# Performance work log

Hardware: AMD Instinct MI355X
Metric: run time of the kernel (lower is better)

## Reference

```python
import jax, jax.numpy as jnp
import numpy as np

N_NODES, N_EDGES = 50000, 800000
NODE_D, MSG_D, OUT_D = 128, 128, 128


def _linear_params(key, d_in, d_out):
    kw, _ = jax.random.split(key)
    W = jax.random.normal(kw, (d_in, d_out), jnp.float32) * np.float32(1.0 / np.sqrt(d_in))
    b = jnp.zeros((d_out,), jnp.float32)
    return W, b


def setup_inputs() -> dict:
    key = jax.random.key(0)
    ks = jax.random.split(key, 12)
    node_features = jax.random.normal(ks[0], (N_NODES, NODE_D), jnp.float32)
    src = jax.random.randint(ks[1], (N_EDGES,), 0, N_NODES, dtype=jnp.int32)
    dst = jax.random.randint(ks[2], (N_EDGES,), 0, N_NODES, dtype=jnp.int32)
    W_msg_1, b_msg_1 = _linear_params(ks[3], NODE_D, MSG_D)
    W_msg_2, b_msg_2 = _linear_params(ks[4], MSG_D, MSG_D)
    W_msg_3, b_msg_3 = _linear_params(ks[5], MSG_D, MSG_D)
    W_att_1, b_att_1 = _linear_params(ks[6], 2 * NODE_D, 1)
    W_att_2, b_att_2 = _linear_params(ks[7], 2 * NODE_D, 1)
    W_att_3, b_att_3 = _linear_params(ks[8], 2 * NODE_D, 1)
    W_c1, b_c1 = _linear_params(ks[9], MSG_D + NODE_D, OUT_D)
    W_c2, b_c2 = _linear_params(ks[10], OUT_D, OUT_D)
    return {
        'node_features': node_features, 'src': src, 'dst': dst,
        'W_msg_1': W_msg_1, 'b_msg_1': b_msg_1,
        'W_msg_2': W_msg_2, 'b_msg_2': b_msg_2,
        'W_msg_3': W_msg_3, 'b_msg_3': b_msg_3,
        'W_att_1': W_att_1, 'b_att_1': b_att_1,
        'W_att_2': W_att_2, 'b_att_2': b_att_2,
        'W_att_3': W_att_3, 'b_att_3': b_att_3,
        'W_c1': W_c1, 'b_c1': b_c1,
        'W_c2': W_c2, 'b_c2': b_c2,
    }


def reference(node_features, src, dst,
              W_msg_1, b_msg_1, W_msg_2, b_msg_2, W_msg_3, b_msg_3,
              W_att_1, b_att_1, W_att_2, b_att_2, W_att_3, b_att_3,
              W_c1, b_c1, W_c2, b_c2):
    # dropout(0.2) is identity in eval mode
    h = node_features                     # [N, D]
    N = h.shape[0]
    hs = h[src]                           # [E, D] gather source features
    hd = h[dst]                           # [E, D] gather dest features
    e = jnp.concatenate([hs, hd], axis=1)  # [E, 2D]

    # three per-edge scalar attention heads: exp(relu(linear))
    a1 = jnp.exp(jax.nn.relu(e @ W_att_1 + b_att_1))  # [E, 1]
    a2 = jnp.exp(jax.nn.relu(e @ W_att_2 + b_att_2))
    a3 = jnp.exp(jax.nn.relu(e @ W_att_3 + b_att_3))

    # per-destination normalizers (segment sums over incoming edges)
    att1 = jax.ops.segment_sum(a1, dst, num_segments=N)  # [N, 1]
    att2 = jax.ops.segment_sum(a2, dst, num_segments=N)
    att3 = jax.ops.segment_sum(a3, dst, num_segments=N)

    avg_a = (a1 / att1[dst] + a2 / att2[dst] + a3 / att3[dst]) / 3.0  # [E, 1]

    # gathered 3-layer MLP message, scaled by averaged attention
    m = avg_a * jax.nn.relu(
        jax.nn.relu(jax.nn.relu(hs @ W_msg_1 + b_msg_1) @ W_msg_2 + b_msg_2) @ W_msg_3 + b_msg_3
    )  # [E, M]

    # mean over incoming edges (nodes with no in-edges get 0, like DGL)
    deg = jax.ops.segment_sum(jnp.ones((src.shape[0], 1), h.dtype), dst, num_segments=N)
    h_neigh = jax.ops.segment_sum(m, dst, num_segments=N) / jnp.maximum(deg, 1.0)  # [N, M]

    hc = jnp.concatenate([h, h_neigh], axis=1)  # [N, D+M]
    out = jax.nn.relu(hc @ W_c1 + b_c1) @ W_c2 + b_c2  # [N, O]
    return out
```

## Files before the change

### kernel.cpp

```cpp
#include <hip/hip_runtime.h>

#define NDIM 128
#define NBKT 512
#define NWPART 128

typedef __attribute__((ext_vector_type(8))) short s8v;
typedef __attribute__((ext_vector_type(4))) float f4v;

__device__ inline unsigned short f2bf_rne(float x) {
    unsigned u = __float_as_uint(x);
    unsigned r = u + 0x7FFFu + ((u >> 16) & 1u);
    return (unsigned short)(r >> 16);
}
__device__ inline float bf2f(unsigned short b) {
    return __uint_as_float(((unsigned)b) << 16);
}

__global__ __launch_bounds__(256) void k_front(const float* __restrict__ h,
                                               const float* __restrict__ Wa1,
                                               const float* __restrict__ Wa2,
                                               const float* __restrict__ Wa3,
                                               float* __restrict__ proj,
                                               unsigned short* __restrict__ hb,
                                               const float* __restrict__ w0,
                                               const float* __restrict__ w1,
                                               const float* __restrict__ w2,
                                               const float* __restrict__ w3,
                                               const float* __restrict__ w4,
                                               const float* __restrict__ w5,
                                               unsigned short* __restrict__ wtout,
                                               const int* __restrict__ dst,
                                               int* __restrict__ hist,
                                               int N, int E, int npb)
{
    __shared__ int lh[NBKT];
    int tid = threadIdx.x;
    int nbProj = (N + 15) >> 4;
    int bid = blockIdx.x;

    if (bid < 384) {
        const float* srcs[6] = {w0, w1, w2, w3, w4, w5};
        int mat = bid >> 6;
        int idx = (bid & 63) * 256 + tid;
        int j    = idx & 7;
        int lane = (idx >> 3) & 63;
        int ks   = (idx >> 9) & 3;
        int ct   = idx >> 11;
        int col  = ct * 16 + (lane & 15);
        int k    = ks * 32 + (lane >> 4) * 8 + j;
        wtout[(size_t)mat * 16384 + idx] = f2bf_rne(srcs[mat][k * 128 + col]);
        return;
    }
    bid -= 384;
    if (bid < nbProj) {
        int l = tid & 15;
        int n = bid * 16 + (tid >> 4);
        if (n >= N) return;
        int o = l * 8;
        float4 w1s0 = *(const float4*)(Wa1 + o),       w1s1 = *(const float4*)(Wa1 + o + 4);
        float4 w1d0 = *(const float4*)(Wa1 + 128 + o), w1d1 = *(const float4*)(Wa1 + 132 + o);
        float4 w2s0 = *(const float4*)(Wa2 + o),       w2s1 = *(const float4*)(Wa2 + o + 4);
        float4 w2d0 = *(const float4*)(Wa2 + 128 + o), w2d1 = *(const float4*)(Wa2 + 132 + o);
        float4 w3s0 = *(const float4*)(Wa3 + o),       w3s1 = *(const float4*)(Wa3 + o + 4);
        float4 w3d0 = *(const float4*)(Wa3 + 128 + o), w3d1 = *(const float4*)(Wa3 + 132 + o);
        float4 x0 = *(const float4*)(h + (size_t)n * NDIM + o);
        float4 x1 = *(const float4*)(h + (size_t)n * NDIM + o + 4);
        {
            s8v hv;
            hv[0] = (short)f2bf_rne(x0.x); hv[1] = (short)f2bf_rne(x0.y);
            hv[2] = (short)f2bf_rne(x0.z); hv[3] = (short)f2bf_rne(x0.w);
            hv[4] = (short)f2bf_rne(x1.x); hv[5] = (short)f2bf_rne(x1.y);
            hv[6] = (short)f2bf_rne(x1.z); hv[7] = (short)f2bf_rne(x1.w);
            *(s8v*)(hb + (size_t)n * NDIM + o) = hv;
        }
        float s1 = x0.x*w1s0.x + x0.y*w1s0.y + x0.z*w1s0.z + x0.w*w1s0.w
                 + x1.x*w1s1.x + x1.y*w1s1.y + x1.z*w1s1.z + x1.w*w1s1.w;
        float s2 = x0.x*w2s0.x + x0.y*w2s0.y + x0.z*w2s0.z + x0.w*w2s0.w
                 + x1.x*w2s1.x + x1.y*w2s1.y + x1.z*w2s1.z + x1.w*w2s1.w;
        float s3 = x0.x*w3s0.x + x0.y*w3s0.y + x0.z*w3s0.z + x0.w*w3s0.w
                 + x1.x*w3s1.x + x1.y*w3s1.y + x1.z*w3s1.z + x1.w*w3s1.w;
        float d1 = x0.x*w1d0.x + x0.y*w1d0.y + x0.z*w1d0.z + x0.w*w1d0.w
                 + x1.x*w1d1.x + x1.y*w1d1.y + x1.z*w1d1.z + x1.w*w1d1.w;
        float d2 = x0.x*w2d0.x + x0.y*w2d0.y + x0.z*w2d0.z + x0.w*w2d0.w
                 + x1.x*w2d1.x + x1.y*w2d1.y + x1.z*w2d1.z + x1.w*w2d1.w;
        float d3 = x0.x*w3d0.x + x0.y*w3d0.y + x0.z*w3d0.z + x0.w*w3d0.w
                 + x1.x*w3d1.x + x1.y*w3d1.y + x1.z*w3d1.z + x1.w*w3d1.w;
#pragma unroll
        for (int m = 1; m < 16; m <<= 1) {
            s1 += __shfl_xor(s1, m);
            s2 += __shfl_xor(s2, m);
            s3 += __shfl_xor(s3, m);
            d1 += __shfl_xor(d1, m);
            d2 += __shfl_xor(d2, m);
            d3 += __shfl_xor(d3, m);
        }
        if (l == 0) {
            *(float4*)(proj + (size_t)n * 8)     = make_float4(s1, s2, s3, 0.f);
            *(float4*)(proj + (size_t)n * 8 + 4) = make_float4(d1, d2, d3, 0.f);
        }
        return;
    }
    bid -= nbProj;
    {
        int w = bid, NW = NWPART;
        for (int i = tid; i < NBKT; i += 256) lh[i] = 0;
        __syncthreads();
        int per = (E + NW - 1) / NW;
        int e0 = w * per, e1 = min(E, e0 + per);
        for (int e = e0 + tid; e < e1; e += 256)
            atomicAdd(&lh[dst[e] / npb], 1);
        __syncthreads();
        for (int b = tid; b < NBKT; b += 256)
            hist[b * NW + w] = lh[b];
    }
}

__global__ __launch_bounds__(NWPART) void k_pscan_a(int* __restrict__ hist,
                                                    int* __restrict__ tot)
{
    __shared__ int s[NWPART];
    int b = blockIdx.x, t = threadIdx.x;
    int v = hist[b * NWPART + t];
    s[t] = v;
    __syncthreads();
    for (int d = 1; d < NWPART; d <<= 1) {
        int u = (t >= d) ? s[t - d] : 0;
        __syncthreads();
        s[t] += u;
        __syncthreads();
    }
    hist[b * NWPART + t] = s[t] - v;
    if (t == NWPART - 1) tot[b] = s[NWPART - 1];
}

__global__ __launch_bounds__(NBKT) void k_pscan_b(const int* __restrict__ tot,
                                                  int* __restrict__ bbase, int E)
{
    __shared__ int s[NBKT];
    int b = threadIdx.x;
    int v = tot[b];
    s[b] = v;
    __syncthreads();
    for (int d = 1; d < NBKT; d <<= 1) {
        int u = (b >= d) ? s[b - d] : 0;
        __syncthreads();
        s[b] += u;
        __syncthreads();
    }
    bbase[b] = s[b] - v;
    if (b == NBKT - 1) bbase[NBKT] = E;
}


__device__ inline void g_pass_global(const unsigned short* __restrict__ A, int N, int row0,
                                     int ln, int g, int lane, int cw,
                                     const unsigned short* __restrict__ wf, f4v acc[2][2])
{
#pragma unroll
    for (int ks = 0; ks < 4; ++ks) {
        s8v a[2];
#pragma unroll
        for (int fr = 0; fr < 2; ++fr) {
            int rA = min(row0 + fr * 16 + ln, N - 1);
            a[fr] = *(const s8v*)(A + (size_t)rA * 128 + ks * 32 + g * 8);
        }
#pragma unroll
        for (int ct2 = 0; ct2 < 2; ++ct2) {
            int ct = cw * 2 + ct2;
            s8v wv = *(const s8v*)(wf + ((((ct << 2) + ks) * 64) + lane) * 8);
#pragma unroll
            for (int fr = 0; fr < 2; ++fr)
                acc[fr][ct2] = __builtin_amdgcn_mfma_f32_16x16x32_bf16(a[fr], wv, acc[fr][ct2], 0, 0, 0);
        }
    }
}

__device__ inline void g_pass_lds(const unsigned short* __restrict__ act,
                                  int rw, int ln, int g, int lane, int cw,
                                  const unsigned short* __restrict__ wf, f4v acc[2][2])
{
#pragma unroll
    for (int ks = 0; ks < 4; ++ks) {
        s8v a[2];
#pragma unroll
        for (int fr = 0; fr < 2; ++fr) {
            int rl = rw * 32 + fr * 16 + ln;
            a[fr] = *(const s8v*)(&act[(rl * 128 + ks * 32 + g * 8) ^ ((ln & 7) << 3)]);
        }
#pragma unroll
        for (int ct2 = 0; ct2 < 2; ++ct2) {
            int ct = cw * 2 + ct2;
            s8v wv = *(const s8v*)(wf + ((((ct << 2) + ks) * 64) + lane) * 8);
#pragma unroll
            for (int fr = 0; fr < 2; ++fr)
                acc[fr][ct2] = __builtin_amdgcn_mfma_f32_16x16x32_bf16(a[fr], wv, acc[fr][ct2], 0, 0, 0);
        }
    }
}

__device__ inline void write_act(f4v acc[2][2], const float* __restrict__ bias,
                                 unsigned short* __restrict__ act,
                                 int rw, int cw, int ln, int g)
{
#pragma unroll
    for (int ct2 = 0; ct2 < 2; ++ct2) {
        int col = (cw * 2 + ct2) * 16 + ln;
        float bv = bias[col];
#pragma unroll
        for (int fr = 0; fr < 2; ++fr) {
#pragma unroll
            for (int q = 0; q < 4; ++q) {
                int rl = rw * 32 + fr * 16 + g * 4 + q;
                float o = fmaxf(acc[fr][ct2][q] + bv, 0.f);
                act[(rl * 128 + col) ^ ((rl & 7) << 3)] = f2bf_rne(o);
                acc[fr][ct2][q] = 0.f;
            }
        }
    }
}

__global__ __launch_bounds__(512) void k_mid(const int* __restrict__ src,
                                             const int* __restrict__ dst,
                                             const int* __restrict__ hist,
                                             const int* __restrict__ bbase,
                                             unsigned* __restrict__ ebuf,
                                             int E, int npb,
                                             const unsigned short* __restrict__ hb,
                                             const unsigned short* __restrict__ w1,
                                             const unsigned short* __restrict__ w2,
                                             const unsigned short* __restrict__ w3,
                                             const float* __restrict__ b1,
                                             const float* __restrict__ b2,
                                             const float* __restrict__ b3,
                                             unsigned short* __restrict__ msg, int N)
{
    __shared__ int cur[NBKT];
    __shared__ unsigned short act0[8192];
    __shared__ unsigned short act1[8192];
    int tid = threadIdx.x;

    if (blockIdx.x < NWPART) {
        int w = blockIdx.x, NW = NWPART;
        for (int i = tid; i < NBKT; i += 512)
            cur[i] = hist[i * NW + w] + bbase[i];
        __syncthreads();
        int per = (E + NW - 1) / NW;
        int e0 = w * per, e1 = min(E, e0 + per);
        for (int e = e0 + tid; e < e1; e += 512) {
            int d = dst[e], b = d / npb;
            int pos = atomicAdd(&cur[b], 1);
            ebuf[pos] = ((unsigned)src[e] << 7) | (unsigned)(d - b * npb);
        }
        return;
    }
    int mb   = blockIdx.x - NWPART;
    int lane = tid & 63;
    int wid  = tid >> 6;
    int rw   = wid >> 2;
    int cw   = wid & 3;
    int ln   = lane & 15;
    int g    = lane >> 4;
    int row0 = mb * 64 + rw * 32;

    f4v acc[2][2] = {};
    g_pass_global(hb, N, row0, ln, g, lane, cw, w1, acc);
    write_act(acc, b1, act0, rw, cw, ln, g);
    __syncthreads();
    g_pass_lds(act0, rw, ln, g, lane, cw, w2, acc);
    write_act(acc, b2, act1, rw, cw, ln, g);
    __syncthreads();
    g_pass_lds(act1, rw, ln, g, lane, cw, w3, acc);
    write_act(acc, b3, act0, rw, cw, ln, g);
    __syncthreads();
#pragma unroll
    for (int i = 0; i < 2; ++i) {
        int id  = tid + 512 * i;
        int row = id >> 4;
        int c8  = (id & 15) * 8;
        int grow = mb * 64 + row;
        if (grow < N) {
            s8v v = *(const s8v*)(&act0[(row * 128 + c8) ^ ((row & 7) << 3)]);
            *(s8v*)(msg + (size_t)grow * 128 + c8) = v;
        }
    }
}

__global__ __launch_bounds__(256) void k_bucket(const unsigned* __restrict__ ebuf,
                                                const int* __restrict__ bbase,
                                                int* __restrict__ offs,
                                                int* __restrict__ perm,
                                                int N, int npb, int E)
{
    __shared__ int lc[128];
    __shared__ int ls[128];
    int b   = blockIdx.x;
    int tid = threadIdx.x;
    for (int i = tid; i < 128; i += 256) lc[i] = 0;
    __syncthreads();
    int e0 = bbase[b], e1 = bbase[b + 1];
    for (int e = e0 + tid; e < e1; e += 256)
        atomicAdd(&lc[ebuf[e] & 127], 1);
    __syncthreads();
    if (tid < 128) ls[tid] = lc[tid];
    __syncthreads();
    for (int d = 1; d < 128; d <<= 1) {
        int u = (tid < 128 && tid >= d) ? ls[tid - d] : 0;
        __syncthreads();
        if (tid < 128) ls[tid] += u;
        __syncthreads();
    }
    int n0 = b * npb;
    if (tid < 128) {
        int excl = ls[tid] - lc[tid] + e0;
        if (tid < npb && n0 + tid < N) offs[n0 + tid] = excl;
        lc[tid] = excl;
    }
    if (b == 0 && tid == 0) offs[N] = E;
    __syncthreads();
    for (int e = e0 + tid; e < e1; e += 256) {
        unsigned r = ebuf[e];
        int pos = atomicAdd(&lc[r & 127], 1);
        perm[pos] = (int)(r >> 7);
    }
}

__global__ __launch_bounds__(512) void k_tail(const unsigned short* __restrict__ hb,
                                              const unsigned short* __restrict__ msgb,
                                              const float* __restrict__ proj,
                                              const int* __restrict__ offs,
                                              const int* __restrict__ perm,
                                              const float* __restrict__ ba1,
                                              const float* __restrict__ ba2,
                                              const float* __restrict__ ba3,
                                              const unsigned short* __restrict__ wc1a,
                                              const unsigned short* __restrict__ wc1b,
                                              const unsigned short* __restrict__ wc2,
                                              const float* __restrict__ bc1,
                                              const float* __restrict__ bc2,
                                              float* __restrict__ out, int N)
{
    __shared__ unsigned short hn[8192];
    __shared__ unsigned short act0[8192];
    int tid  = threadIdx.x;
    int lane = tid & 63;
    int l    = lane & 15;
    int grp  = lane >> 4;
    int wv   = tid >> 6;
    int r0   = blockIdx.x * 64;
    float b1 = ba1[0], b2 = ba2[0], b3 = ba3[0];

    for (int rnd = 0; rnd < 2; ++rnd) {
        int rl = rnd * 32 + wv * 4 + grp;
        int n  = r0 + rl;
        bool alive = (n < N);
        int o0 = 0, o1 = 0;
        float dd1 = 0.f, dd2 = 0.f, dd3 = 0.f;
        if (alive) {
            o0 = offs[n];
            o1 = offs[n + 1];
            dd1 = proj[(size_t)n * 8 + 4];
            dd2 = proj[(size_t)n * 8 + 5];
            dd3 = proj[(size_t)n * 8 + 6];
        }
        int deg = o1 - o0;

        int   m0 = min(deg, 16);
        int   sc = 0;
        float a1c = 0.f, a2c = 0.f, a3c = 0.f;
        if (l < m0) {
            sc = perm[o0 + l];
            float4 sp = *(const float4*)(proj + (size_t)sc * 8);
            a1c = __expf(fmaxf(sp.x + dd1 + b1, 0.f));
            a2c = __expf(fmaxf(sp.y + dd2 + b2, 0.f));
            a3c = __expf(fmaxf(sp.z + dd3 + b3, 0.f));
        }
        float s1 = a1c, s2 = a2c, s3 = a3c;
        for (int i = o0 + 16 + l; i < o1; i += 16) {
            int s = perm[i];
            float4 sp = *(const float4*)(proj + (size_t)s * 8);
            s1 += __expf(fmaxf(sp.x + dd1 + b1, 0.f));
            s2 += __expf(fmaxf(sp.y + dd2 + b2, 0.f));
            s3 += __expf(fmaxf(sp.z + dd3 + b3, 0.f));
        }
#pragma unroll
        for (int m = 1; m < 16; m <<= 1) {
            s1 += __shfl_xor(s1, m);
            s2 += __shfl_xor(s2, m);
            s3 += __shfl_xor(s3, m);
        }
        float r1 = 1.f / s1, r2 = 1.f / s2, r3 = 1.f / s3;

        float acc[8] = {};
        int gbase = grp << 4;
        {
            float wvv = (a1c * r1 + a2c * r2 + a3c * r3) * (1.f / 3.f);
            for (int j = 0; j < m0; ++j) {
                int   s = __shfl(sc, gbase + j);
                float w = __shfl(wvv, gbase + j);
                s8v v = *(const s8v*)(msgb + (size_t)s * NDIM + l * 8);
#pragma unroll
                for (int k = 0; k < 8; ++k)
                    acc[k] += w * bf2f((unsigned short)v[k]);
            }
        }
        for (int base = o0 + 16; base < o1; base += 16) {
            int m  = min(16, o1 - base);
            int sv = 0;
            float wvv = 0.f;
            if (l < m) {
                sv = perm[base + l];
                float4 sp = *(const float4*)(proj + (size_t)sv * 8);
                float a1 = __expf(fmaxf(sp.x + dd1 + b1, 0.f));
                float a2 = __expf(fmaxf(sp.y + dd2 + b2, 0.f));
                float a3 = __expf(fmaxf(sp.z + dd3 + b3, 0.f));
                wvv = (a1 * r1 + a2 * r2 + a3 * r3) * (1.f / 3.f);
            }
            for (int j = 0; j < m; ++j) {
                int   s = __shfl(sv, gbase + j);
                float w = __shfl(wvv, gbase + j);
                s8v v = *(const s8v*)(msgb + (size_t)s * NDIM + l * 8);
#pragma unroll
                for (int k = 0; k < 8; ++k)
                    acc[k] += w * bf2f((unsigned short)v[k]);
            }
        }
        float inv = (alive && deg > 0) ? 1.f / (float)deg : 0.f;
        s8v hv;
#pragma unroll
        for (int k = 0; k < 8; ++k)
            hv[k] = (short)f2bf_rne(acc[k] * inv);
        *(s8v*)(&hn[(rl * 128 + l * 8) ^ ((rl & 7) << 3)]) = hv;
    }
    __syncthreads();

    int wid  = tid >> 6;
    int rw   = wid >> 2;
    int cw   = wid & 3;
    int ln   = lane & 15;
    int g    = lane >> 4;
    int row0 = r0 + rw * 32;

    f4v acc2[2][2] = {};
    g_pass_global(hb, N, row0, ln, g, lane, cw, wc1a, acc2);
    g_pass_lds(hn, rw, ln, g, lane, cw, wc1b, acc2);
    write_act(acc2, bc1, act0, rw, cw, ln, g);
    __syncthreads();
    g_pass_lds(act0, rw, ln, g, lane, cw, wc2, acc2);
#pragma unroll
    for (int ct2 = 0; ct2 < 2; ++ct2) {
        int col = (cw * 2 + ct2) * 16 + ln;
        float bv = bc2[col];
#pragma unroll
        for (int fr = 0; fr < 2; ++fr) {
#pragma unroll
            for (int q = 0; q < 4; ++q) {
                int orow = row0 + fr * 16 + g * 4 + q;
                if (orow < N)
                    out[(size_t)orow * 128 + col] = acc2[fr][ct2][q] + bv;
            }
        }
    }
}

extern "C" void kernel_launch(void* const* d_in, const int* in_sizes, int n_in,
                              void* d_out, int out_size, void* d_ws, size_t ws_size,
                              hipStream_t stream)
{
    const float* h   = (const float*)d_in[0];
    const int*   src = (const int*)d_in[1];
    const int*   dst = (const int*)d_in[2];
    const float* Wm1 = (const float*)d_in[3];
    const float* bm1 = (const float*)d_in[4];
    const float* Wm2 = (const float*)d_in[5];
    const float* bm2 = (const float*)d_in[6];
    const float* Wm3 = (const float*)d_in[7];
    const float* bm3 = (const float*)d_in[8];
    const float* Wa1 = (const float*)d_in[9];
    const float* ba1 = (const float*)d_in[10];
    const float* Wa2 = (const float*)d_in[11];
    const float* ba2 = (const float*)d_in[12];
    const float* Wa3 = (const float*)d_in[13];
    const float* ba3 = (const float*)d_in[14];
    const float* Wc1 = (const float*)d_in[15];
    const float* bc1 = (const float*)d_in[16];
    const float* Wc2 = (const float*)d_in[17];
    const float* bc2 = (const float*)d_in[18];

    const int N = in_sizes[0] / NDIM;
    const int E = in_sizes[1];
    const int npb = (N + NBKT - 1) / NBKT;
    float* out = (float*)d_out;

    unsigned short* wt  = (unsigned short*)d_ws;
    unsigned short* hb  = wt + 6 * 16384;
    unsigned short* mb2 = hb + (size_t)N * NDIM;
    float* proj = (float*)(mb2 + (size_t)N * NDIM);
    int* offs   = (int*)(proj + (size_t)N * 8);
    int* hist   = offs + N + 1;
    int* bbase  = hist + NBKT * NWPART;
    int* btot   = bbase + NBKT + 1;
    unsigned* ebuf = (unsigned*)(btot + NBKT);
    int* perm   = (int*)(ebuf + E);

    const unsigned short* wt_m1  = wt;
    const unsigned short* wt_m2  = wt + 1 * 16384;
    const unsigned short* wt_m3  = wt + 2 * 16384;
    const unsigned short* wt_c1a = wt + 3 * 16384;
    const unsigned short* wt_c1b = wt + 4 * 16384;
    const unsigned short* wt_c2  = wt + 5 * 16384;

    int nbProj = (N + 15) / 16;
    int gb64   = (N + 63) / 64;

    k_front<<<384 + nbProj + NWPART, 256, 0, stream>>>(
        h, Wa1, Wa2, Wa3, proj, hb,
        Wm1, Wm2, Wm3, Wc1, Wc1 + 128 * 128, Wc2, wt,
        dst, hist, N, E, npb);

    k_pscan_a<<<NBKT, NWPART, 0, stream>>>(hist, btot);
    k_pscan_b<<<1, NBKT, 0, stream>>>(btot, bbase, E);

    k_mid<<<NWPART + gb64, 512, 0, stream>>>(
        src, dst, hist, bbase, ebuf, E, npb,
        hb, wt_m1, wt_m2, wt_m3, bm1, bm2, bm3, mb2, N);

    k_bucket<<<NBKT, 256, 0, stream>>>(ebuf, bbase, offs, perm, N, npb, E);

    k_tail<<<gb64, 512, 0, stream>>>(
        hb, mb2, proj, offs, perm, ba1, ba2, ba3,
        wt_c1a, wt_c1b, wt_c2, bc1, bc2, out, N);
}
```

Before: 108.7 us.

## Align dst buckets to 64-node tiles and fuse per-node sort into tail kernel

```diff
diff --git a/kernel.cpp b/kernel.cpp
--- a/kernel.cpp
+++ b/kernel.cpp
@@ -1,8 +1,8 @@
 #include <hip/hip_runtime.h>
 
 #define NDIM 128
-#define NBKT 512
 #define NWPART 128
+#define MAXBKT 1024
 
 typedef __attribute__((ext_vector_type(8))) short s8v;
 typedef __attribute__((ext_vector_type(4))) float f4v;
@@ -31,9 +31,9 @@
                                                unsigned short* __restrict__ wtout,
                                                const int* __restrict__ dst,
                                                int* __restrict__ hist,
-                                               int N, int E, int npb)
-{
-    __shared__ int lh[NBKT];
+                                               int N, int E, int nbkt)
+{
+    __shared__ int lh[MAXBKT];
     int tid = threadIdx.x;
     int nbProj = (N + 15) >> 4;
     int bid = blockIdx.x;
@@ -103,14 +103,14 @@
     bid -= nbProj;
     {
         int w = bid, NW = NWPART;
-        for (int i = tid; i < NBKT; i += 256) lh[i] = 0;
+        for (int i = tid; i < nbkt; i += 256) lh[i] = 0;
         __syncthreads();
         int per = (E + NW - 1) / NW;
         int e0 = w * per, e1 = min(E, e0 + per);
         for (int e = e0 + tid; e < e1; e += 256)
-            atomicAdd(&lh[dst[e] / npb], 1);
-        __syncthreads();
-        for (int b = tid; b < NBKT; b += 256)
+            atomicAdd(&lh[dst[e] >> 6], 1);
+        __syncthreads();
+        for (int b = tid; b < nbkt; b += 256)
             hist[b * NW + w] = lh[b];
     }
 }
@@ -133,22 +133,23 @@
     if (t == NWPART - 1) tot[b] = s[NWPART - 1];
 }
 
-__global__ __launch_bounds__(NBKT) void k_pscan_b(const int* __restrict__ tot,
-                                                  int* __restrict__ bbase, int E)
-{
-    __shared__ int s[NBKT];
+__global__ __launch_bounds__(MAXBKT) void k_pscan_b(const int* __restrict__ tot,
+                                                    int* __restrict__ bbase,
+                                                    int E, int nbkt)
+{
+    __shared__ int s[MAXBKT];
     int b = threadIdx.x;
-    int v = tot[b];
+    int v = (b < nbkt) ? tot[b] : 0;
     s[b] = v;
     __syncthreads();
-    for (int d = 1; d < NBKT; d <<= 1) {
+    for (int d = 1; d < MAXBKT; d <<= 1) {
         int u = (b >= d) ? s[b - d] : 0;
         __syncthreads();
         s[b] += u;
         __syncthreads();
     }
-    bbase[b] = s[b] - v;
-    if (b == NBKT - 1) bbase[NBKT] = E;
+    if (b < nbkt) bbase[b] = s[b] - v;
+    if (b == nbkt - 1) bbase[nbkt] = E;
 }
 
 
@@ -224,7 +225,7 @@
                                              const int* __restrict__ hist,
                                              const int* __restrict__ bbase,
                                              unsigned* __restrict__ ebuf,
-                                             int E, int npb,
+                                             int E, int nbkt,
                                              const unsigned short* __restrict__ hb,
                                              const unsigned short* __restrict__ w1,
                                              const unsigned short* __restrict__ w2,
@@ -234,22 +235,22 @@
                                              const float* __restrict__ b3,
                                              unsigned short* __restrict__ msg, int N)
 {
-    __shared__ int cur[NBKT];
+    __shared__ int cur[MAXBKT];
     __shared__ unsigned short act0[8192];
     __shared__ unsigned short act1[8192];
     int tid = threadIdx.x;
 
     if (blockIdx.x < NWPART) {
         int w = blockIdx.x, NW = NWPART;
-        for (int i = tid; i < NBKT; i += 512)
+        for (int i = tid; i < nbkt; i += 512)
             cur[i] = hist[i * NW + w] + bbase[i];
         __syncthreads();
         int per = (E + NW - 1) / NW;
         int e0 = w * per, e1 = min(E, e0 + per);
         for (int e = e0 + tid; e < e1; e += 512) {
-            int d = dst[e], b = d / npb;
+            int d = dst[e], b = d >> 6;
             int pos = atomicAdd(&cur[b], 1);
-            ebuf[pos] = ((unsigned)src[e] << 7) | (unsigned)(d - b * npb);
+            ebuf[pos] = ((unsigned)src[e] << 7) | (unsigned)(d & 63);
         }
         return;
     }
@@ -285,50 +286,11 @@
     }
 }
 
-__global__ __launch_bounds__(256) void k_bucket(const unsigned* __restrict__ ebuf,
-                                                const int* __restrict__ bbase,
-                                                int* __restrict__ offs,
-                                                int* __restrict__ perm,
-                                                int N, int npb, int E)
-{
-    __shared__ int lc[128];
-    __shared__ int ls[128];
-    int b   = blockIdx.x;
-    int tid = threadIdx.x;
-    for (int i = tid; i < 128; i += 256) lc[i] = 0;
-    __syncthreads();
-    int e0 = bbase[b], e1 = bbase[b + 1];
-    for (int e = e0 + tid; e < e1; e += 256)
-        atomicAdd(&lc[ebuf[e] & 127], 1);
-    __syncthreads();
-    if (tid < 128) ls[tid] = lc[tid];
-    __syncthreads();
-    for (int d = 1; d < 128; d <<= 1) {
-        int u = (tid < 128 && tid >= d) ? ls[tid - d] : 0;
-        __syncthreads();
-        if (tid < 128) ls[tid] += u;
-        __syncthreads();
-    }
-    int n0 = b * npb;
-    if (tid < 128) {
-        int excl = ls[tid] - lc[tid] + e0;
-        if (tid < npb && n0 + tid < N) offs[n0 + tid] = excl;
-        lc[tid] = excl;
-    }
-    if (b == 0 && tid == 0) offs[N] = E;
-    __syncthreads();
-    for (int e = e0 + tid; e < e1; e += 256) {
-        unsigned r = ebuf[e];
-        int pos = atomicAdd(&lc[r & 127], 1);
-        perm[pos] = (int)(r >> 7);
-    }
-}
-
 __global__ __launch_bounds__(512) void k_tail(const unsigned short* __restrict__ hb,
                                               const unsigned short* __restrict__ msgb,
                                               const float* __restrict__ proj,
-                                              const int* __restrict__ offs,
-                                              const int* __restrict__ perm,
+                                              const int* __restrict__ bbase,
+                                              const unsigned* __restrict__ ebuf,
                                               const float* __restrict__ ba1,
                                               const float* __restrict__ ba2,
                                               const float* __restrict__ ba3,
@@ -341,6 +303,11 @@
 {
     __shared__ unsigned short hn[8192];
     __shared__ unsigned short act0[8192];
+    __shared__ int lperm[1536];
+    __shared__ int lcnt[64];
+    __shared__ int lsc[64];
+    __shared__ int loffs[65];
+    __shared__ int lcur[64];
     int tid  = threadIdx.x;
     int lane = tid & 63;
     int l    = lane & 15;
@@ -349,15 +316,41 @@
     int r0   = blockIdx.x * 64;
     float b1 = ba1[0], b2 = ba2[0], b3 = ba3[0];
 
+    int be0 = bbase[blockIdx.x], be1 = bbase[blockIdx.x + 1];
+    if (tid < 64) lcnt[tid] = 0;
+    __syncthreads();
+    for (int e = be0 + tid; e < be1; e += 512)
+        atomicAdd(&lcnt[ebuf[e] & 63], 1);
+    __syncthreads();
+    if (tid < 64) lsc[tid] = lcnt[tid];
+    __syncthreads();
+    for (int d = 1; d < 64; d <<= 1) {
+        int u = (tid < 64 && tid >= d) ? lsc[tid - d] : 0;
+        __syncthreads();
+        if (tid < 64) lsc[tid] += u;
+        __syncthreads();
+    }
+    if (tid < 64) {
+        int excl = lsc[tid] - lcnt[tid];
+        loffs[tid] = excl;
+        lcur[tid]  = excl;
+        if (tid == 63) loffs[64] = lsc[63];
+    }
+    __syncthreads();
+    for (int e = be0 + tid; e < be1; e += 512) {
+        unsigned r = ebuf[e];
+        int p = atomicAdd(&lcur[r & 63], 1);
+        if (p < 1536) lperm[p] = (int)(r >> 7);
+    }
+    __syncthreads();
+
     for (int rnd = 0; rnd < 2; ++rnd) {
         int rl = rnd * 32 + wv * 4 + grp;
         int n  = r0 + rl;
         bool alive = (n < N);
-        int o0 = 0, o1 = 0;
+        int o0 = loffs[rl], o1 = loffs[rl + 1];
         float dd1 = 0.f, dd2 = 0.f, dd3 = 0.f;
         if (alive) {
-            o0 = offs[n];
-            o1 = offs[n + 1];
             dd1 = proj[(size_t)n * 8 + 4];
             dd2 = proj[(size_t)n * 8 + 5];
             dd3 = proj[(size_t)n * 8 + 6];
@@ -368,7 +361,7 @@
         int   sc = 0;
         float a1c = 0.f, a2c = 0.f, a3c = 0.f;
         if (l < m0) {
-            sc = perm[o0 + l];
+            sc = lperm[o0 + l];
             float4 sp = *(const float4*)(proj + (size_t)sc * 8);
             a1c = __expf(fmaxf(sp.x + dd1 + b1, 0.f));
             a2c = __expf(fmaxf(sp.y + dd2 + b2, 0.f));
@@ -376,7 +369,7 @@
         }
         float s1 = a1c, s2 = a2c, s3 = a3c;
         for (int i = o0 + 16 + l; i < o1; i += 16) {
-            int s = perm[i];
+            int s = lperm[i];
             float4 sp = *(const float4*)(proj + (size_t)s * 8);
             s1 += __expf(fmaxf(sp.x + dd1 + b1, 0.f));
             s2 += __expf(fmaxf(sp.y + dd2 + b2, 0.f));
@@ -408,7 +401,7 @@
             int sv = 0;
             float wvv = 0.f;
             if (l < m) {
-                sv = perm[base + l];
+                sv = lperm[base + l];
                 float4 sp = *(const float4*)(proj + (size_t)sv * 8);
                 float a1 = __expf(fmaxf(sp.x + dd1 + b1, 0.f));
                 float a2 = __expf(fmaxf(sp.y + dd2 + b2, 0.f));
@@ -488,19 +481,17 @@
 
     const int N = in_sizes[0] / NDIM;
     const int E = in_sizes[1];
-    const int npb = (N + NBKT - 1) / NBKT;
+    const int nbkt = (N + 63) >> 6;
     float* out = (float*)d_out;
 
     unsigned short* wt  = (unsigned short*)d_ws;
     unsigned short* hb  = wt + 6 * 16384;
     unsigned short* mb2 = hb + (size_t)N * NDIM;
     float* proj = (float*)(mb2 + (size_t)N * NDIM);
-    int* offs   = (int*)(proj + (size_t)N * 8);
-    int* hist   = offs + N + 1;
-    int* bbase  = hist + NBKT * NWPART;
-    int* btot   = bbase + NBKT + 1;
-    unsigned* ebuf = (unsigned*)(btot + NBKT);
-    int* perm   = (int*)(ebuf + E);
+    int* hist   = (int*)(proj + (size_t)N * 8);
+    int* bbase  = hist + MAXBKT * NWPART;
+    int* btot   = bbase + MAXBKT + 1;
+    unsigned* ebuf = (unsigned*)(btot + MAXBKT);
 
     const unsigned short* wt_m1  = wt;
     const unsigned short* wt_m2  = wt + 1 * 16384;
@@ -510,23 +501,21 @@
     const unsigned short* wt_c2  = wt + 5 * 16384;
 
     int nbProj = (N + 15) / 16;
-    int gb64   = (N + 63) / 64;
+    int gb64   = nbkt;
 
     k_front<<<384 + nbProj + NWPART, 256, 0, stream>>>(
         h, Wa1, Wa2, Wa3, proj, hb,
         Wm1, Wm2, Wm3, Wc1, Wc1 + 128 * 128, Wc2, wt,
-        dst, hist, N, E, npb);
-
-    k_pscan_a<<<NBKT, NWPART, 0, stream>>>(hist, btot);
-    k_pscan_b<<<1, NBKT, 0, stream>>>(btot, bbase, E);
+        dst, hist, N, E, nbkt);
+
+    k_pscan_a<<<nbkt, NWPART, 0, stream>>>(hist, btot);
+    k_pscan_b<<<1, MAXBKT, 0, stream>>>(btot, bbase, E, nbkt);
 
     k_mid<<<NWPART + gb64, 512, 0, stream>>>(
-        src, dst, hist, bbase, ebuf, E, npb,
+        src, dst, hist, bbase, ebuf, E, nbkt,
         hb, wt_m1, wt_m2, wt_m3, bm1, bm2, bm3, mb2, N);
 
-    k_bucket<<<NBKT, 256, 0, stream>>>(ebuf, bbase, offs, perm, N, npb, E);
-
     k_tail<<<gb64, 512, 0, stream>>>(
-        hb, mb2, proj, offs, perm, ba1, ba2, ba3,
+        hb, mb2, proj, bbase, ebuf, ba1, ba2, ba3,
         wt_c1a, wt_c1b, wt_c2, bc1, bc2, out, N);
 }
```

After: 101.1 us. 7.0% less time.
